# Kernel optimization log

Measured on AMD Instinct MI355X. Metric: run time of the kernel, lower is better.

## Reference

```python
import jax, jax.numpy as jnp
import numpy as np

B, S, HID = 2, 1024, 2048
H, D, KV = 32, 64, 8          # query heads, head dim, kv heads (GQA)
INNER = H * D                 # 2048
KV_DIM = KV * D               # 512


def setup_inputs() -> dict:
    key = jax.random.key(0)
    ks = jax.random.split(key, 12)
    s = 0.02
    return {
        "query": jax.random.normal(ks[0], (B, S, HID), jnp.float32),
        "key": jax.random.normal(ks[1], (B, S, HID), jnp.float32),
        "value": jax.random.normal(ks[2], (B, S, HID), jnp.float32),
        "mask": jnp.zeros((B, 1, S, S), jnp.float32),
        "position_bias": jax.random.normal(ks[3], (1, H, S, S), jnp.float32),
        "Wq": jax.random.normal(ks[4], (HID, INNER), jnp.float32) * s,
        "bq": jnp.zeros((INNER,), jnp.float32),
        "Wk": jax.random.normal(ks[5], (HID, KV_DIM), jnp.float32) * s,
        "bk": jnp.zeros((KV_DIM,), jnp.float32),
        "Wv": jax.random.normal(ks[6], (HID, KV_DIM), jnp.float32) * s,
        "bv": jnp.zeros((KV_DIM,), jnp.float32),
        "Wo": jax.random.normal(ks[7], (INNER, HID), jnp.float32) * s,
        "bo": jnp.zeros((HID,), jnp.float32),
    }


def reference(query, key, value, mask, position_bias, Wq, bq, Wk, bk, Wv, bv, Wo, bo):
    # projections (torch nn.Linear equivalent, weights stored [in,out])
    q = (query @ Wq + bq).reshape(B, S, H, D)     # [B,S,H,D]
    k = (key @ Wk + bk).reshape(B, S, KV, D)      # [B,S,KV,D]
    v = (value @ Wv + bv).reshape(B, S, KV, D)
    rep = H // KV
    k = jnp.repeat(k, rep, axis=2)                # GQA repeat_kv -> [B,S,H,D]
    v = jnp.repeat(v, rep, axis=2)
    scores = jnp.einsum("bqhd,bkhd->bhqk", q, k)  # [B,H,S,S]
    scores = (scores + position_bias) * (1.0 / jnp.sqrt(jnp.float32(D)))
    scores = scores + mask
    probs = jax.nn.softmax(scores.astype(jnp.float32), axis=-1).astype(q.dtype)
    out = jnp.einsum("bhqk,bkhd->bqhd", probs, v).reshape(B, S, INNER)
    return out @ Wo + bo                          # [B,S,HID]
```

## Files before the change

### kernel.cpp

```cpp
#include <hip/hip_runtime.h>
#include <stdint.h>

#define DEVI __device__ __forceinline__

typedef __attribute__((ext_vector_type(8))) short bf16x8;
typedef __attribute__((ext_vector_type(4))) float f32x4;
typedef __attribute__((ext_vector_type(4))) float flt4;
typedef __attribute__((ext_vector_type(8))) unsigned short u16x8;
typedef __attribute__((ext_vector_type(4))) unsigned short u16x4;

DEVI unsigned short f2bf(float f){
  union{float f;uint32_t u;}v; v.f=f;
  uint32_t u=v.u;
  u += 0x7FFFu + ((u>>16)&1u);
  return (unsigned short)(u>>16);
}

DEVI uint32_t cvt_pk_bf16(float lo, float hi){
  uint32_t r;
  asm("v_cvt_pk_bf16_f32 %0, %1, %2" : "=v"(r) : "v"(lo), "v"(hi));
  return r;
}

DEVI float fexp2(float x){
#if __has_builtin(__builtin_amdgcn_exp2f)
  return __builtin_amdgcn_exp2f(x);
#else
  return exp2f(x);
#endif
}

DEVI void gload16(const void* g, void* l){
  __builtin_amdgcn_global_load_lds((const __attribute__((address_space(1))) void*)g,
                                   (__attribute__((address_space(3))) void*)l, 16, 0, 0);
}

__global__ void cvt3_k(const float* __restrict__ q, const float* __restrict__ k,
                       const float* __restrict__ v, unsigned short* __restrict__ qb,
                       unsigned short* __restrict__ kb, unsigned short* __restrict__ vb, int n8){
  int i = blockIdx.x*256 + threadIdx.x;
  if (i >= n8) return;
  const float* src = blockIdx.y==0 ? q : (blockIdx.y==1 ? k : v);
  unsigned short* dst = blockIdx.y==0 ? qb : (blockIdx.y==1 ? kb : vb);
  const flt4* s = (const flt4*)src;
  flt4 a = s[2*i], b = s[2*i+1];
  u16x8 o;
  o[0]=f2bf(a.x); o[1]=f2bf(a.y); o[2]=f2bf(a.z); o[3]=f2bf(a.w);
  o[4]=f2bf(b.x); o[5]=f2bf(b.y); o[6]=f2bf(b.z); o[7]=f2bf(b.w);
  ((u16x8*)dst)[i] = o;
}

__global__ void wtrans_all(const float* __restrict__ Wq, const float* __restrict__ Wk,
                           const float* __restrict__ Wv, const float* __restrict__ Wo,
                           unsigned short* __restrict__ WqT, unsigned short* __restrict__ WkT,
                           unsigned short* __restrict__ WvT, unsigned short* __restrict__ WoT){
  __shared__ float tile[64][65];
  const int K = 2048;
  int id = blockIdx.x;
  const float* W; unsigned short* WT; int N, tt;
  if (id < 1024)      { W=Wq; WT=WqT; N=2048; tt=id; }
  else if (id < 1280) { W=Wk; WT=WkT; N=512;  tt=id-1024; }
  else if (id < 1536) { W=Wv; WT=WvT; N=512;  tt=id-1280; }
  else                { W=Wo; WT=WoT; N=2048; tt=id-1536; }
  int sh = (N==2048) ? 5 : 3;
  int n0 = (tt & ((1<<sh)-1))*64, k0 = (tt >> sh)*64;
  int t = threadIdx.x;
  int r = t>>4, c4 = (t&15)*4;
  #pragma unroll
  for (int i=0;i<4;i++){
    flt4 v = *(const flt4*)&W[(size_t)(k0 + r + i*16)*N + n0 + c4];
    tile[r+i*16][c4+0]=v.x; tile[r+i*16][c4+1]=v.y; tile[r+i*16][c4+2]=v.z; tile[r+i*16][c4+3]=v.w;
  }
  __syncthreads();
  #pragma unroll
  for (int i=0;i<4;i++){
    int rn = r + i*16;
    u16x4 o;
    o[0]=f2bf(tile[c4+0][rn]); o[1]=f2bf(tile[c4+1][rn]);
    o[2]=f2bf(tile[c4+2][rn]); o[3]=f2bf(tile[c4+3][rn]);
    *(u16x4*)&WT[(size_t)(n0+rn)*K + k0 + c4] = o;
  }
}

#define GEMM64_KSTEP(A_, BT_, K_)                                              \
    __syncthreads();                                                           \
    _Pragma("unroll")                                                          \
    for (int j=0;j<2;j++){                                                     \
      int cid = (j*4+w)*64 + l;                                                \
      int row = cid>>3, sl = cid&7;                                            \
      int gsl = sl ^ (row&7);                                                  \
      gload16(&A_ [(size_t)(m0+row)*K_ + k0 + gsl*8], &As[(j*4+w)*512]);       \
      gload16(&BT_[(size_t)(n0+row)*K_ + k0 + gsl*8], &Bs[(j*4+w)*512]);       \
    }                                                                          \
    __syncthreads();                                                           \
    _Pragma("unroll")                                                          \
    for (int kk=0;kk<2;kk++){                                                  \
      bf16x8 af[2], bfv[2];                                                    \
      _Pragma("unroll")                                                        \
      for (int mt=0;mt<2;mt++){                                                \
        int row = wr+mt*16+lq;                                                 \
        af[mt] = *(const bf16x8*)&As[row*64 + (((kk*4+lg)^(lq&7))*8)];         \
      }                                                                        \
      _Pragma("unroll")                                                        \
      for (int nt=0;nt<2;nt++){                                                \
        int row = wc+nt*16+lq;                                                 \
        bfv[nt] = *(const bf16x8*)&Bs[row*64 + (((kk*4+lg)^(lq&7))*8)];        \
      }                                                                        \
      _Pragma("unroll")                                                        \
      for (int mt=0;mt<2;mt++)                                                 \
        _Pragma("unroll")                                                      \
        for (int nt=0;nt<2;nt++)                                               \
          acc[mt][nt] = __builtin_amdgcn_mfma_f32_16x16x32_bf16(af[mt], bfv[nt], acc[mt][nt], 0,0,0); \
    }

__global__ __launch_bounds__(256) void qkv64(const unsigned short* __restrict__ qbf,
    const unsigned short* __restrict__ kbf, const unsigned short* __restrict__ vbf,
    const unsigned short* __restrict__ WqT, const unsigned short* __restrict__ WkT,
    const unsigned short* __restrict__ WvT,
    const float* __restrict__ bq, const float* __restrict__ bk, const float* __restrict__ bv,
    unsigned short* __restrict__ Qp, unsigned short* __restrict__ Kp, unsigned short* __restrict__ VTb){
  __shared__ unsigned short As[64*64];
  __shared__ unsigned short Bs[64*64];
  const int K = 2048;
  int id = blockIdx.x;
  const unsigned short *A, *BT; const float* bias; int N, op, tt;
  if (id < 1024)      { op=0; A=qbf; BT=WqT; bias=bq; N=2048; tt=id; }
  else if (id < 1280) { op=1; A=kbf; BT=WkT; bias=bk; N=512;  tt=id-1024; }
  else                { op=2; A=vbf; BT=WvT; bias=bv; N=512;  tt=id-1280; }
  int sh = (N==2048) ? 5 : 3;
  int n0 = (tt & ((1<<sh)-1))*64, m0 = (tt >> sh)*64;
  int t = threadIdx.x, w = t>>6, l = t&63;
  int lq = l&15, lg = l>>4;
  int wr = (w>>1)*32, wc = (w&1)*32;
  f32x4 acc[2][2] = {};
  for (int k0=0;k0<K;k0+=64){
    GEMM64_KSTEP(A, BT, K)
  }
  #pragma unroll
  for (int nt=0;nt<2;nt++){
    int col = n0 + wc + nt*16 + lq;
    float bvl = bias[col];
    #pragma unroll
    for (int mt=0;mt<2;mt++){
      #pragma unroll
      for (int r=0;r<4;r++){
        int row = m0 + wr + mt*16 + lg*4 + r;
        float v = acc[mt][nt][r] + bvl;
        if (op==0)      Qp[(size_t)row*2048 + col] = f2bf(v);
        else if (op==1) Kp[(size_t)row*512 + col] = f2bf(v);
        else {
          int b = row>>10, s = row&1023;
          VTb[((size_t)(b*512 + col)<<10) + s] = f2bf(v);
        }
      }
    }
  }
}

__global__ __launch_bounds__(256) void oproj64(const unsigned short* __restrict__ A,
    const unsigned short* __restrict__ BT, const float* __restrict__ bias,
    float* __restrict__ Cout){
  __shared__ unsigned short As[64*64];
  __shared__ unsigned short Bs[64*64];
  const int K = 2048, N = 2048;
  int n0 = blockIdx.x*64, m0 = blockIdx.y*64;
  int t = threadIdx.x, w = t>>6, l = t&63;
  int lq = l&15, lg = l>>4;
  int wr = (w>>1)*32, wc = (w&1)*32;
  f32x4 acc[2][2] = {};
  for (int k0=0;k0<K;k0+=64){
    GEMM64_KSTEP(A, BT, K)
  }
  #pragma unroll
  for (int nt=0;nt<2;nt++){
    int col = n0 + wc + nt*16 + lq;
    float bvl = bias[col];
    #pragma unroll
    for (int mt=0;mt<2;mt++){
      #pragma unroll
      for (int r=0;r<4;r++){
        int row = m0 + wr + mt*16 + lg*4 + r;
        Cout[(size_t)row*N + col] = acc[mt][nt][r] + bvl;
      }
    }
  }
}

__global__ __launch_bounds__(256,4) void attn_k(const unsigned short* __restrict__ Q,
    const unsigned short* __restrict__ Kp, const unsigned short* __restrict__ VT,
    const float* __restrict__ pbias, const float* __restrict__ mask,
    unsigned short* __restrict__ Oout){
  __shared__ unsigned short Ks[2][4096];
  __shared__ unsigned short VTs[2][4096];
  __shared__ unsigned short Pb[4][1024];
  int t=threadIdx.x, w=t>>6, l=t&63;
  int qt=blockIdx.x, h=blockIdx.y, b=blockIdx.z;
  int kv=h>>2;
  int lq = l&15, lg = l>>4;
  int q0 = qt*64 + w*16;
  bf16x8 qf0, qf1;
  {
    const unsigned short* qp = &Q[((size_t)(b*1024 + q0 + lq))*2048 + h*64 + lg*8];
    qf0 = *(const bf16x8*)qp;
    qf1 = *(const bf16x8*)(qp + 32);
  }
  const float* pbase = &pbias[((size_t)h*1024 + (q0+lq))*1024];
  const float* mbase = &mask [((size_t)b*1024 + (q0+lq))*1024];
  f32x4 oacc[4] = {};
  float psum = 0.f;
  const float L2E   = 1.4426950408889634f;
  const float SCL2E = 0.125f*1.4426950408889634f;
  const float NFM   = -16.0f*1.4426950408889634f;
  unsigned short* pw = &Pb[w][0];
  int swz = (lq&7)<<3;

  flt4 praw[4], mraw[4], comb[4];

#define ATTN_STAGE(buf_, kt_)                                                          \
  _Pragma("unroll")                                                                    \
  for (int j=0;j<2;j++){                                                               \
    int cid = (j*4+w)*64 + l;                                                          \
    int row = cid>>3, sl = cid&7;                                                      \
    int gsl = sl ^ (row&7);                                                            \
    gload16(&Kp[((size_t)(b*1024 + (kt_)*64 + row))*512 + kv*64 + gsl*8], &Ks[buf_][(j*4+w)*512]);          \
    gload16(&VT[((size_t)(b*512 + kv*64 + row))*1024 + (size_t)((kt_)*64 + gsl*8)], &VTs[buf_][(j*4+w)*512]);\
  }

#define ATTN_RAW(kt_)                                                                  \
  _Pragma("unroll")                                                                    \
  for (int nt=0;nt<4;nt++){                                                            \
    praw[nt] = *(const flt4*)&pbase[(kt_)*64 + nt*16 + lg*4];                          \
    mraw[nt] = *(const flt4*)&mbase[(kt_)*64 + nt*16 + lg*4];                          \
  }

#define ATTN_COMBINE()                                                                 \
  _Pragma("unroll")                                                                    \
  for (int nt=0;nt<4;nt++)                                                             \
    _Pragma("unroll")                                                                  \
    for (int r=0;r<4;r++)                                                              \
      comb[nt][r] = fmaf(praw[nt][r], 0.125f, mraw[nt][r] - 16.0f)*L2E;

#define ATTN_COMPUTE(P_)                                                               \
  {                                                                                    \
    f32x4 sacc[4] = {};                                                                \
    __builtin_amdgcn_s_setprio(1);                                                     \
    _Pragma("unroll")                                                                  \
    for (int nt=0;nt<4;nt++){                                                          \
      int row = nt*16 + lq;                                                            \
      bf16x8 kf0 = *(const bf16x8*)&Ks[P_][row*64 + (( lg    ^ (row&7))*8)];           \
      bf16x8 kf1 = *(const bf16x8*)&Ks[P_][row*64 + (((4+lg) ^ (row&7))*8)];           \
      sacc[nt] = __builtin_amdgcn_mfma_f32_16x16x32_bf16(kf0, qf0, sacc[nt], 0,0,0);   \
      sacc[nt] = __builtin_amdgcn_mfma_f32_16x16x32_bf16(kf1, qf1, sacc[nt], 0,0,0);   \
    }                                                                                  \
    __builtin_amdgcn_s_setprio(0);                                                     \
    _Pragma("unroll")                                                                  \
    for (int nt=0;nt<4;nt++){                                                          \
      float p0 = fexp2(fmaf(sacc[nt][0], SCL2E, comb[nt][0]));                         \
      float p1 = fexp2(fmaf(sacc[nt][1], SCL2E, comb[nt][1]));                         \
      float p2 = fexp2(fmaf(sacc[nt][2], SCL2E, comb[nt][2]));                         \
      float p3 = fexp2(fmaf(sacc[nt][3], SCL2E, comb[nt][3]));                         \
      psum += (p0+p1)+(p2+p3);                                                         \
      uint2 pk;                                                                        \
      pk.x = cvt_pk_bf16(p0,p1);                                                       \
      pk.y = cvt_pk_bf16(p2,p3);                                                       \
      *(uint2*)&pw[lq*64 + ((nt*16 + lg*4) ^ swz)] = pk;                               \
    }                                                                                  \
    _Pragma("unroll")                                                                  \
    for (int kk=0;kk<2;kk++){                                                          \
      bf16x8 pa = *(const bf16x8*)&pw[lq*64 + ((kk*32 + lg*8) ^ swz)];                 \
      __builtin_amdgcn_s_setprio(1);                                                   \
      _Pragma("unroll")                                                                \
      for (int nt=0;nt<4;nt++){                                                        \
        int vrow = nt*16 + lq;                                                         \
        bf16x8 vf = *(const bf16x8*)&VTs[P_][vrow*64 + (((kk*4+lg) ^ (vrow&7))*8)];    \
        oacc[nt] = __builtin_amdgcn_mfma_f32_16x16x32_bf16(pa, vf, oacc[nt], 0,0,0);   \
      }                                                                                \
      __builtin_amdgcn_s_setprio(0);                                                   \
    }                                                                                  \
  }

  ATTN_STAGE(0, 0)
  ATTN_RAW(0)
  asm volatile("s_waitcnt vmcnt(8)" ::: "memory");
  __builtin_amdgcn_s_barrier();

  for (int kt=0; kt<16; ++kt){
    int cur = kt&1;
    ATTN_COMBINE()
    if (kt < 15){
      ATTN_STAGE(cur^1, kt+1)
      ATTN_RAW(kt+1)
    }
    ATTN_COMPUTE(cur)
    if (kt < 15){
      asm volatile("s_waitcnt vmcnt(8)" ::: "memory");
      __builtin_amdgcn_s_barrier();
    }
  }

  float lsum = psum;
  lsum += __shfl_xor(lsum, 16);
  lsum += __shfl_xor(lsum, 32);
  #pragma unroll
  for (int r=0;r<4;r++){
    float lr = __shfl(lsum, lg*4 + r);
    float linv = 1.f/lr;
    int qrow = q0 + lg*4 + r;
    #pragma unroll
    for (int nt=0;nt<4;nt++){
      Oout[((size_t)(b*1024 + qrow))*2048 + h*64 + nt*16 + lq] = f2bf(oacc[nt][r]*linv);
    }
  }
#undef ATTN_COMPUTE
#undef ATTN_COMBINE
#undef ATTN_RAW
#undef ATTN_STAGE
}

extern "C" void kernel_launch(void* const* d_in, const int* in_sizes, int n_in,
                              void* d_out, int out_size, void* d_ws, size_t ws_size,
                              hipStream_t stream){
  (void)in_sizes; (void)n_in; (void)out_size; (void)ws_size;
  const float* query = (const float*)d_in[0];
  const float* key   = (const float*)d_in[1];
  const float* value = (const float*)d_in[2];
  const float* mask  = (const float*)d_in[3];
  const float* pbias = (const float*)d_in[4];
  const float* Wq = (const float*)d_in[5];
  const float* bq = (const float*)d_in[6];
  const float* Wk = (const float*)d_in[7];
  const float* bk = (const float*)d_in[8];
  const float* Wv = (const float*)d_in[9];
  const float* bv = (const float*)d_in[10];
  const float* Wo = (const float*)d_in[11];
  const float* bo = (const float*)d_in[12];
  char* ws = (char*)d_ws;
  const size_t MB = (size_t)1<<20;
  unsigned short* qbf = (unsigned short*)(ws + 0*MB);
  unsigned short* kbf = (unsigned short*)(ws + 8*MB);
  unsigned short* vbf = (unsigned short*)(ws + 16*MB);
  unsigned short* WqT = (unsigned short*)(ws + 24*MB);
  unsigned short* WkT = (unsigned short*)(ws + 32*MB);
  unsigned short* WvT = (unsigned short*)(ws + 34*MB);
  unsigned short* WoT = (unsigned short*)(ws + 36*MB);
  unsigned short* Qp  = (unsigned short*)(ws + 44*MB);
  unsigned short* Kp  = (unsigned short*)(ws + 52*MB);
  unsigned short* VTb = (unsigned short*)(ws + 54*MB);
  unsigned short* Aout= (unsigned short*)(ws + 56*MB);

  cvt3_k<<<dim3(2048,3),256,0,stream>>>(query, key, value, qbf, kbf, vbf, 524288);
  wtrans_all<<<2560,256,0,stream>>>(Wq, Wk, Wv, Wo, WqT, WkT, WvT, WoT);
  qkv64<<<1536,256,0,stream>>>(qbf, kbf, vbf, WqT, WkT, WvT, bq, bk, bv, Qp, Kp, VTb);
  attn_k<<<dim3(16,32,2),256,0,stream>>>(Qp, Kp, VTb, pbias, mask, Aout);
  oproj64<<<dim3(32,32),256,0,stream>>>(Aout, WoT, bo, (float*)d_out);
}
```

Before: 183.3 us.

## Group GQA heads per workgroup to share K/V tiles and stage mask in LDS

Each 512-thread workgroup now handles the four query heads of one KV group for 32 query rows, so a K/V tile loaded into LDS is reused across four heads instead of being reloaded per head. The mask tile is loaded once per workgroup into shared memory and shared across heads, and the position-bias loads are double-buffered two tiles ahead in registers. Blocks are remapped with an XCD-aware swizzle of the linear block index. The cost is more LDS, larger workgroups, and extra barriers per tile, which may reduce occupancy.

```diff
diff --git a/kernel.cpp b/kernel.cpp
--- a/kernel.cpp
+++ b/kernel.cpp
@@ -186,26 +186,31 @@
   }
 }
 
-__global__ __launch_bounds__(256,4) void attn_k(const unsigned short* __restrict__ Q,
+__global__ __launch_bounds__(512,4) void attn_k(const unsigned short* __restrict__ Q,
     const unsigned short* __restrict__ Kp, const unsigned short* __restrict__ VT,
     const float* __restrict__ pbias, const float* __restrict__ mask,
     unsigned short* __restrict__ Oout){
   __shared__ unsigned short Ks[2][4096];
   __shared__ unsigned short VTs[2][4096];
-  __shared__ unsigned short Pb[4][1024];
+  __shared__ float Ms[2][2048];
+  __shared__ unsigned short Pb[8][1024];
   int t=threadIdx.x, w=t>>6, l=t&63;
-  int qt=blockIdx.x, h=blockIdx.y, b=blockIdx.z;
-  int kv=h>>2;
+  int phys = blockIdx.x;
+  int lin = (phys&7)*64 + (phys>>3);
+  int qb = lin>>4, kv = (lin>>1)&7, b = lin&1;
+  int h = kv*4 + (w&3);
+  int qhalf = w>>2;
   int lq = l&15, lg = l>>4;
-  int q0 = qt*64 + w*16;
+  int q0 = qb*32 + qhalf*16;
+  int mr = qhalf*16 + lq;
   bf16x8 qf0, qf1;
   {
     const unsigned short* qp = &Q[((size_t)(b*1024 + q0 + lq))*2048 + h*64 + lg*8];
     qf0 = *(const bf16x8*)qp;
     qf1 = *(const bf16x8*)(qp + 32);
   }
-  const float* pbase = &pbias[((size_t)h*1024 + (q0+lq))*1024];
-  const float* mbase = &mask [((size_t)b*1024 + (q0+lq))*1024];
+  const float* pbase  = &pbias[((size_t)h*1024 + (q0+lq))*1024];
+  const float* maskWG = &mask [((size_t)(b*1024 + qb*32))*1024];
   f32x4 oacc[4] = {};
   float psum = 0.f;
   const float L2E   = 1.4426950408889634f;
@@ -214,89 +219,93 @@
   unsigned short* pw = &Pb[w][0];
   int swz = (lq&7)<<3;
 
-  flt4 praw[4], mraw[4], comb[4];
-
-#define ATTN_STAGE(buf_, kt_)                                                          \
-  _Pragma("unroll")                                                                    \
-  for (int j=0;j<2;j++){                                                               \
-    int cid = (j*4+w)*64 + l;                                                          \
-    int row = cid>>3, sl = cid&7;                                                      \
-    int gsl = sl ^ (row&7);                                                            \
-    gload16(&Kp[((size_t)(b*1024 + (kt_)*64 + row))*512 + kv*64 + gsl*8], &Ks[buf_][(j*4+w)*512]);          \
-    gload16(&VT[((size_t)(b*512 + kv*64 + row))*1024 + (size_t)((kt_)*64 + gsl*8)], &VTs[buf_][(j*4+w)*512]);\
-  }
-
-#define ATTN_RAW(kt_)                                                                  \
-  _Pragma("unroll")                                                                    \
-  for (int nt=0;nt<4;nt++){                                                            \
-    praw[nt] = *(const flt4*)&pbase[(kt_)*64 + nt*16 + lg*4];                          \
-    mraw[nt] = *(const flt4*)&mbase[(kt_)*64 + nt*16 + lg*4];                          \
-  }
-
-#define ATTN_COMBINE()                                                                 \
-  _Pragma("unroll")                                                                    \
-  for (int nt=0;nt<4;nt++)                                                             \
-    _Pragma("unroll")                                                                  \
-    for (int r=0;r<4;r++)                                                              \
-      comb[nt][r] = fmaf(praw[nt][r], 0.125f, mraw[nt][r] - 16.0f)*L2E;
-
-#define ATTN_COMPUTE(P_)                                                               \
-  {                                                                                    \
-    f32x4 sacc[4] = {};                                                                \
-    __builtin_amdgcn_s_setprio(1);                                                     \
-    _Pragma("unroll")                                                                  \
-    for (int nt=0;nt<4;nt++){                                                          \
-      int row = nt*16 + lq;                                                            \
-      bf16x8 kf0 = *(const bf16x8*)&Ks[P_][row*64 + (( lg    ^ (row&7))*8)];           \
-      bf16x8 kf1 = *(const bf16x8*)&Ks[P_][row*64 + (((4+lg) ^ (row&7))*8)];           \
-      sacc[nt] = __builtin_amdgcn_mfma_f32_16x16x32_bf16(kf0, qf0, sacc[nt], 0,0,0);   \
-      sacc[nt] = __builtin_amdgcn_mfma_f32_16x16x32_bf16(kf1, qf1, sacc[nt], 0,0,0);   \
-    }                                                                                  \
-    __builtin_amdgcn_s_setprio(0);                                                     \
-    _Pragma("unroll")                                                                  \
-    for (int nt=0;nt<4;nt++){                                                          \
-      float p0 = fexp2(fmaf(sacc[nt][0], SCL2E, comb[nt][0]));                         \
-      float p1 = fexp2(fmaf(sacc[nt][1], SCL2E, comb[nt][1]));                         \
-      float p2 = fexp2(fmaf(sacc[nt][2], SCL2E, comb[nt][2]));                         \
-      float p3 = fexp2(fmaf(sacc[nt][3], SCL2E, comb[nt][3]));                         \
-      psum += (p0+p1)+(p2+p3);                                                         \
-      uint2 pk;                                                                        \
-      pk.x = cvt_pk_bf16(p0,p1);                                                       \
-      pk.y = cvt_pk_bf16(p2,p3);                                                       \
-      *(uint2*)&pw[lq*64 + ((nt*16 + lg*4) ^ swz)] = pk;                               \
-    }                                                                                  \
-    _Pragma("unroll")                                                                  \
-    for (int kk=0;kk<2;kk++){                                                          \
-      bf16x8 pa = *(const bf16x8*)&pw[lq*64 + ((kk*32 + lg*8) ^ swz)];                 \
-      __builtin_amdgcn_s_setprio(1);                                                   \
-      _Pragma("unroll")                                                                \
-      for (int nt=0;nt<4;nt++){                                                        \
-        int vrow = nt*16 + lq;                                                         \
-        bf16x8 vf = *(const bf16x8*)&VTs[P_][vrow*64 + (((kk*4+lg) ^ (vrow&7))*8)];    \
-        oacc[nt] = __builtin_amdgcn_mfma_f32_16x16x32_bf16(pa, vf, oacc[nt], 0,0,0);   \
-      }                                                                                \
-      __builtin_amdgcn_s_setprio(0);                                                   \
-    }                                                                                  \
+  flt4 RA[4], RB[4], comb[4];
+
+#define ATTN_STAGE(buf_, kt_)                                                           \
+  {                                                                                     \
+    int c = w*64 + l;                                                                   \
+    int krow = c>>3, ksl = (c&7)^(krow&7);                                              \
+    gload16(&Kp[((size_t)(b*1024 + (kt_)*64 + krow))*512 + kv*64 + ksl*8], &Ks[buf_][w*512]);          \
+    gload16(&VT[((size_t)(b*512 + kv*64 + krow))*1024 + (size_t)((kt_)*64 + ksl*8)], &VTs[buf_][w*512]);\
+    int mrow = c>>4, msl = (c&15)^(mrow&7);                                             \
+    gload16(&maskWG[(size_t)mrow*1024 + (kt_)*64 + msl*4], &Ms[buf_][w*256]);           \
+  }
+
+#define ATTN_RAW(RP_, kt_)                                                              \
+  _Pragma("unroll")                                                                     \
+  for (int nt=0;nt<4;nt++)                                                              \
+    RP_[nt] = *(const flt4*)&pbase[(kt_)*64 + nt*16 + lg*4];
+
+#define ATTN_COMBINE(RP_, cur_)                                                         \
+  _Pragma("unroll")                                                                     \
+  for (int nt=0;nt<4;nt++){                                                             \
+    flt4 m4 = *(const flt4*)&Ms[cur_][mr*64 + (((nt*4+lg)^(mr&7))<<2)];                 \
+    _Pragma("unroll")                                                                   \
+    for (int r=0;r<4;r++)                                                               \
+      comb[nt][r] = fmaf(RP_[nt][r], SCL2E, fmaf(m4[r], L2E, NFM));                     \
+  }
+
+#define ATTN_COMPUTE(P_)                                                                \
+  {                                                                                     \
+    f32x4 sacc[4] = {};                                                                 \
+    __builtin_amdgcn_s_setprio(1);                                                      \
+    _Pragma("unroll")                                                                   \
+    for (int nt=0;nt<4;nt++){                                                           \
+      int row = nt*16 + lq;                                                             \
+      bf16x8 kf0 = *(const bf16x8*)&Ks[P_][row*64 + (( lg    ^ (row&7))*8)];            \
+      bf16x8 kf1 = *(const bf16x8*)&Ks[P_][row*64 + (((4+lg) ^ (row&7))*8)];            \
+      sacc[nt] = __builtin_amdgcn_mfma_f32_16x16x32_bf16(kf0, qf0, sacc[nt], 0,0,0);    \
+      sacc[nt] = __builtin_amdgcn_mfma_f32_16x16x32_bf16(kf1, qf1, sacc[nt], 0,0,0);    \
+    }                                                                                   \
+    __builtin_amdgcn_s_setprio(0);                                                      \
+    _Pragma("unroll")                                                                   \
+    for (int nt=0;nt<4;nt++){                                                           \
+      float p0 = fexp2(fmaf(sacc[nt][0], SCL2E, comb[nt][0]));                          \
+      float p1 = fexp2(fmaf(sacc[nt][1], SCL2E, comb[nt][1]));                          \
+      float p2 = fexp2(fmaf(sacc[nt][2], SCL2E, comb[nt][2]));                          \
+      float p3 = fexp2(fmaf(sacc[nt][3], SCL2E, comb[nt][3]));                          \
+      psum += (p0+p1)+(p2+p3);                                                          \
+      uint2 pk;                                                                         \
+      pk.x = cvt_pk_bf16(p0,p1);                                                        \
+      pk.y = cvt_pk_bf16(p2,p3);                                                        \
+      *(uint2*)&pw[lq*64 + ((nt*16 + lg*4) ^ swz)] = pk;                                \
+    }                                                                                   \
+    _Pragma("unroll")                                                                   \
+    for (int kk=0;kk<2;kk++){                                                           \
+      bf16x8 pa = *(const bf16x8*)&pw[lq*64 + ((kk*32 + lg*8) ^ swz)];                  \
+      __builtin_amdgcn_s_setprio(1);                                                    \
+      _Pragma("unroll")                                                                 \
+      for (int nt=0;nt<4;nt++){                                                         \
+        int vrow = nt*16 + lq;                                                          \
+        bf16x8 vf = *(const bf16x8*)&VTs[P_][vrow*64 + (((kk*4+lg) ^ (vrow&7))*8)];     \
+        oacc[nt] = __builtin_amdgcn_mfma_f32_16x16x32_bf16(pa, vf, oacc[nt], 0,0,0);    \
+      }                                                                                 \
+      __builtin_amdgcn_s_setprio(0);                                                    \
+    }                                                                                   \
+  }
+
+#define TILE(kt_, cur_, RP_, DOSTAGE, DORAW, VMFULL)                                    \
+  {                                                                                     \
+    if (DOSTAGE) ATTN_STAGE((cur_)^1, (kt_)+1)                                          \
+    if (VMFULL) { asm volatile("s_waitcnt vmcnt(7)" ::: "memory"); }                    \
+    else        { asm volatile("s_waitcnt vmcnt(0)" ::: "memory"); }                    \
+    __builtin_amdgcn_s_barrier();                                                       \
+    ATTN_COMBINE(RP_, cur_)                                                             \
+    if (DORAW) ATTN_RAW(RP_, (kt_)+2)                                                   \
+    ATTN_COMPUTE(cur_)                                                                  \
+    __builtin_amdgcn_s_barrier();                                                       \
   }
 
   ATTN_STAGE(0, 0)
-  ATTN_RAW(0)
-  asm volatile("s_waitcnt vmcnt(8)" ::: "memory");
-  __builtin_amdgcn_s_barrier();
-
-  for (int kt=0; kt<16; ++kt){
-    int cur = kt&1;
-    ATTN_COMBINE()
-    if (kt < 15){
-      ATTN_STAGE(cur^1, kt+1)
-      ATTN_RAW(kt+1)
-    }
-    ATTN_COMPUTE(cur)
-    if (kt < 15){
-      asm volatile("s_waitcnt vmcnt(8)" ::: "memory");
-      __builtin_amdgcn_s_barrier();
-    }
-  }
+  ATTN_RAW(RA, 0)
+  ATTN_RAW(RB, 1)
+
+  for (int kb=0; kb<14; kb+=2){
+    TILE(kb+0, 0, RA, 1, 1, 1)
+    TILE(kb+1, 1, RB, 1, 1, 1)
+  }
+  TILE(14, 0, RA, 1, 0, 1)
+  TILE(15, 1, RB, 0, 0, 0)
 
   float lsum = psum;
   lsum += __shfl_xor(lsum, 16);
@@ -311,6 +320,7 @@
       Oout[((size_t)(b*1024 + qrow))*2048 + h*64 + nt*16 + lq] = f2bf(oacc[nt][r]*linv);
     }
   }
+#undef TILE
 #undef ATTN_COMPUTE
 #undef ATTN_COMBINE
 #undef ATTN_RAW
@@ -351,6 +361,6 @@
   cvt3_k<<<dim3(2048,3),256,0,stream>>>(query, key, value, qbf, kbf, vbf, 524288);
   wtrans_all<<<2560,256,0,stream>>>(Wq, Wk, Wv, Wo, WqT, WkT, WvT, WoT);
   qkv64<<<1536,256,0,stream>>>(qbf, kbf, vbf, WqT, WkT, WvT, bq, bk, bv, Qp, Kp, VTb);
-  attn_k<<<dim3(16,32,2),256,0,stream>>>(Qp, Kp, VTb, pbias, mask, Aout);
+  attn_k<<<512,512,0,stream>>>(Qp, Kp, VTb, pbias, mask, Aout);
   oproj64<<<dim3(32,32),256,0,stream>>>(Aout, WoT, bo, (float*)d_out);
 }
```

After: 153.7 us. -16.1%, faster.
